# Kernel optimization log

Hardware: AMD Instinct MI355X
Metric: run time of the kernel (lower is better)

Reference implementation:

```python
import jax, jax.numpy as jnp
import numpy as np


def setup_inputs() -> dict:
    key = jax.random.key(0)
    ks = jax.random.split(key, 4)
    B, H, W, C = 4, 64, 64, 256
    Ck = C // 8
    x = jax.random.normal(ks[0], (B, H, W, C), dtype=jnp.float32)
    Wf = jax.random.normal(ks[1], (C, Ck), dtype=jnp.float32) * (1.0 / np.sqrt(C))
    Wg = jax.random.normal(ks[2], (C, Ck), dtype=jnp.float32) * (1.0 / np.sqrt(C))
    Wh = jax.random.normal(ks[3], (C, C), dtype=jnp.float32) * (1.0 / np.sqrt(C))
    bf = jnp.zeros((Ck,), jnp.float32)
    bg = jnp.zeros((Ck,), jnp.float32)
    bh = jnp.zeros((C,), jnp.float32)
    gamma = jnp.ones((1,), jnp.float32)
    return {"x": x, "Wf": Wf, "bf": bf, "Wg": Wg, "bg": bg, "Wh": Wh, "bh": bh, "gamma": gamma}


def reference(x, Wf, bf, Wg, bg, Wh, bh, gamma):
    B, H, W, C = x.shape
    N = H * W
    xf = x.reshape(B, N, C)  # hw_flatten; 1x1 conv == per-pixel matmul
    f = xf @ Wf + bf          # [B, N, C//8] (keys)
    g = xf @ Wg + bg          # [B, N, C//8] (queries)
    h = xf @ Wh + bh          # [B, N, C]    (values)
    s = jnp.einsum('bnk,bmk->bnm', g, f)   # [B, N, N], no scaling (as in source)
    b = jax.nn.softmax(s, axis=-1)
    o = jnp.einsum('bnm,bmc->bnc', b, h)   # [B, N, C]
    y = gamma * o.reshape(B, H, W, C) + x
    return y
```

## Files before the change

kernel.cpp:

```cpp
#include <hip/hip_runtime.h>
#include <stdint.h>

typedef short short8 __attribute__((ext_vector_type(8)));
typedef short short4_t __attribute__((ext_vector_type(4)));
typedef float f32x4 __attribute__((ext_vector_type(4)));

__device__ __forceinline__ float bf2f(unsigned short u) {
    union { unsigned int i; float f; } v; v.i = ((unsigned int)u) << 16; return v.f;
}
__device__ __forceinline__ unsigned short f2bf(float f) {
    union { float f; unsigned int i; } v; v.f = f;
    return (unsigned short)((v.i + 0x8000u) >> 16);
}

__global__ __launch_bounds__(256) void k_pre(const float* __restrict__ x,
                                             const float* __restrict__ Wf,
                                             const float* __restrict__ Wg,
                                             const float* __restrict__ Wh,
                                             unsigned short* __restrict__ xh,
                                             unsigned short* __restrict__ xl,
                                             unsigned short* __restrict__ wTh,
                                             unsigned short* __restrict__ wTl) {
    if (blockIdx.x < 2048) {
        int gid = blockIdx.x * 256 + threadIdx.x;
        const float* src = x + (size_t)gid * 8;
        f32x4 a0 = *(const f32x4*)src;
        f32x4 a1 = *(const f32x4*)(src + 4);
        short8 sh, sl;
#pragma unroll
        for (int j = 0; j < 4; ++j) {
            unsigned short h0 = f2bf(a0[j]);
            sh[j] = (short)h0; sl[j] = (short)f2bf(a0[j] - bf2f(h0));
            unsigned short h1 = f2bf(a1[j]);
            sh[4 + j] = (short)h1; sl[4 + j] = (short)f2bf(a1[j] - bf2f(h1));
        }
        *(short8*)&xh[(size_t)gid * 8] = sh;
        *(short8*)&xl[(size_t)gid * 8] = sl;
    } else {
        int col = blockIdx.x - 2048;
        int k = threadIdx.x;
        float v;
        if (col < 32) v = Wf[k * 32 + col];
        else if (col < 64) v = Wg[k * 32 + (col - 32)];
        else v = Wh[k * 256 + (col - 64)];
        unsigned short h = f2bf(v);
        wTh[col * 256 + k] = h;
        if (col < 64) wTl[col * 256 + k] = f2bf(v - bf2f(h));
    }
}

__global__ __launch_bounds__(256) void k_proj(
    const unsigned short* __restrict__ xh,
    const unsigned short* __restrict__ xl,
    const unsigned short* __restrict__ wTh,
    const unsigned short* __restrict__ wTl,
    const float* __restrict__ bfb,
    const float* __restrict__ bgb,
    const float* __restrict__ bhb,
    unsigned short* __restrict__ fKh,
    unsigned short* __restrict__ fKl,
    unsigned short* __restrict__ gQh,
    unsigned short* __restrict__ gQl,
    unsigned short* __restrict__ hT) {
    __shared__ short sm[4 * 64 * 72];
    int tid = threadIdx.x;
    int wave = tid >> 6, lane = tid & 63, lq = lane & 15, quad = lane >> 4;
    int rt = blockIdx.x;
    const unsigned short* xhb = xh + (size_t)rt * 64 * 256;
    const unsigned short* xlb = xl + (size_t)rt * 64 * 256;
    f32x4 zero4 = {0.f, 0.f, 0.f, 0.f};

    if (blockIdx.y < 4) {
        const int XO = 0, WO = 64 * 136;
        int cb = blockIdx.y;
        const unsigned short* wbase = wTh + (size_t)(64 + cb * 64) * 256;
        f32x4 acc[4] = {zero4, zero4, zero4, zero4};

        for (int ph = 0; ph < 2; ++ph) {
            int k0 = ph * 128;
            __syncthreads();
#pragma unroll
            for (int u = 0; u < 4; ++u) {
                int q = u * 256 + tid;
                int row = q >> 4, kc = q & 15;
                *(short8*)&sm[XO + row * 136 + kc * 8] =
                    *(const short8*)&xhb[row * 256 + k0 + kc * 8];
                *(short8*)&sm[WO + row * 136 + kc * 8] =
                    *(const short8*)&wbase[row * 256 + k0 + kc * 8];
            }
            __syncthreads();
#pragma unroll
            for (int ks = 0; ks < 4; ++ks) {
                short8 a = *(const short8*)&sm[XO + (wave * 16 + lq) * 136 + ks * 32 + quad * 8];
#pragma unroll
                for (int ct = 0; ct < 4; ++ct) {
                    short8 bfr = *(const short8*)&sm[WO + (lq + 16 * ct) * 136 + ks * 32 + quad * 8];
                    acc[ct] = __builtin_amdgcn_mfma_f32_16x16x32_bf16(a, bfr, acc[ct], 0, 0, 0);
                }
            }
        }

        int rowl = wave * 16 + quad * 4;
        int grow0 = rt * 64;
        int bidx = grow0 >> 12, n0 = (grow0 & 4095) + rowl;
#pragma unroll
        for (int ct = 0; ct < 4; ++ct) {
            int c = cb * 64 + lq + 16 * ct;
            float bias = bhb[c];
            short4_t pk;
#pragma unroll
            for (int r = 0; r < 4; ++r) pk[r] = (short)f2bf(acc[ct][r] + bias);
            size_t a8 = (((size_t)(bidx * 16 + (c >> 4)) * 128 + (n0 >> 5)) * 64 +
                         ((n0 & 31) >> 3) * 16 + (c & 15)) * 8 + (n0 & 7);
            *(short4_t*)&hT[a8] = pk;
        }
    } else {
        const int XH = 0, XL = 64 * 72, WH = 2 * 64 * 72, WL = 3 * 64 * 72;
        f32x4 acc[4] = {zero4, zero4, zero4, zero4};

        for (int ph = 0; ph < 4; ++ph) {
            int k0 = ph * 64;
            __syncthreads();
#pragma unroll
            for (int u = 0; u < 2; ++u) {
                int q = u * 256 + tid;
                int row = q >> 3, kc = q & 7;
                *(short8*)&sm[XH + row * 72 + kc * 8] =
                    *(const short8*)&xhb[row * 256 + k0 + kc * 8];
                *(short8*)&sm[XL + row * 72 + kc * 8] =
                    *(const short8*)&xlb[row * 256 + k0 + kc * 8];
                *(short8*)&sm[WH + row * 72 + kc * 8] =
                    *(const short8*)&wTh[row * 256 + k0 + kc * 8];
                *(short8*)&sm[WL + row * 72 + kc * 8] =
                    *(const short8*)&wTl[row * 256 + k0 + kc * 8];
            }
            __syncthreads();
#pragma unroll
            for (int ks = 0; ks < 2; ++ks) {
                short8 ah = *(const short8*)&sm[XH + (wave * 16 + lq) * 72 + ks * 32 + quad * 8];
                short8 al = *(const short8*)&sm[XL + (wave * 16 + lq) * 72 + ks * 32 + quad * 8];
#pragma unroll
                for (int ct = 0; ct < 4; ++ct) {
                    short8 bh = *(const short8*)&sm[WH + (lq + 16 * ct) * 72 + ks * 32 + quad * 8];
                    short8 bl = *(const short8*)&sm[WL + (lq + 16 * ct) * 72 + ks * 32 + quad * 8];
                    acc[ct] = __builtin_amdgcn_mfma_f32_16x16x32_bf16(ah, bh, acc[ct], 0, 0, 0);
                    acc[ct] = __builtin_amdgcn_mfma_f32_16x16x32_bf16(al, bh, acc[ct], 0, 0, 0);
                    acc[ct] = __builtin_amdgcn_mfma_f32_16x16x32_bf16(ah, bl, acc[ct], 0, 0, 0);
                }
            }
        }

        int rowl = wave * 16 + quad * 4;
#pragma unroll
        for (int ct = 0; ct < 4; ++ct) {
            int coll = lq + 16 * ct;
#pragma unroll
            for (int r = 0; r < 4; ++r) {
                int grow = rt * 64 + rowl + r;
                int bidx = grow >> 12, n = grow & 4095;
                float v = acc[ct][r];
                size_t o = (size_t)(bidx * 256 + (n >> 4)) * 512 +
                           (((coll & 31) >> 3) * 16 + (n & 15)) * 8 + (coll & 7);
                if (coll < 32) {
                    v += bfb[coll];
                    unsigned short h = f2bf(v);
                    fKh[o] = h;
                    fKl[o] = f2bf(v - bf2f(h));
                } else {
                    int cg = coll - 32;
                    size_t og = (size_t)(bidx * 256 + (n >> 4)) * 512 +
                                ((cg >> 3) * 16 + (n & 15)) * 8 + (cg & 7);
                    v += bgb[cg];
                    unsigned short h = f2bf(v);
                    gQh[og] = h;
                    gQl[og] = f2bf(v - bf2f(h));
                }
            }
        }
    }
}

#define PSTR 72
__global__ __launch_bounds__(256, 2) void k_attn(
    const unsigned short* __restrict__ fKh,
    const unsigned short* __restrict__ fKl,
    const unsigned short* __restrict__ gQh,
    const unsigned short* __restrict__ gQl,
    const unsigned short* __restrict__ hT,
    float* __restrict__ pacc0,
    float* __restrict__ pacc1,
    float* __restrict__ pl0,
    float* __restrict__ pl1) {
    __shared__ short Ps[2][64 * PSTR];
    __shared__ short Fb[2][2][2048];
    int tid = threadIdx.x;
    int wave = tid >> 6, lane = tid & 63, lq = lane & 15, quad = lane >> 4;
    int b = blockIdx.x & 3;
    int rest = blockIdx.x >> 2;
    int qt = rest & 63;
    int ks = rest >> 6;

    const unsigned short* fhB = fKh + (size_t)b * 131072;
    const unsigned short* flB = fKl + (size_t)b * 131072;
    const unsigned short* hB  = hT + (size_t)b * 1048576;
    float* pacc = ks ? pacc1 : pacc0;
    float* pl   = ks ? pl1 : pl0;

    int qrow0 = qt * 64 + wave * 16;
    int lchunk = quad * 16 + lq;

    f32x4 zero4 = {0.f, 0.f, 0.f, 0.f};
    f32x4 acc[16];
#pragma unroll
    for (int i = 0; i < 16; ++i) acc[i] = zero4;
    float l_part[4] = {0.f, 0.f, 0.f, 0.f};

    int gtile = b * 256 + qt * 4 + wave;
    short8 ghfrag = *(const short8*)&gQh[(size_t)gtile * 512 + lchunk * 8];
    short8 glfrag = *(const short8*)&gQl[(size_t)gtile * 512 + lchunk * 8];

    int ft0 = ks * 128;
    *(short8*)&Fb[0][0][tid * 8] = *(const short8*)&fhB[(size_t)ft0 * 512 + tid * 8];
    *(short8*)&Fb[0][1][tid * 8] = *(const short8*)&flB[(size_t)ft0 * 512 + tid * 8];
    __syncthreads();

    for (int kt = 0; kt < 32; ++kt) {
        int p = kt & 1;
        int nft = ft0 + (kt < 31 ? (kt + 1) * 4 : kt * 4);
        short8 fnh = *(const short8*)&fhB[(size_t)nft * 512 + tid * 8];
        short8 fnl = *(const short8*)&flB[(size_t)nft * 512 + tid * 8];

        int k0 = ks * 64 + kt * 2;
        short8 hb[4][2];
#pragma unroll
        for (int ct = 0; ct < 4; ++ct) {
            int ctile = wave * 4 + ct;
#pragma unroll
            for (int kk = 0; kk < 2; ++kk)
                hb[ct][kk] = *(const short8*)
                    &hB[(((size_t)ctile * 128 + k0 + kk) * 64 + lchunk) * 8];
        }

        f32x4 S[4];
#pragma unroll
        for (int t = 0; t < 4; ++t) {
            short8 fh = *(const short8*)&Fb[p][0][t * 512 + lchunk * 8];
            short8 fl = *(const short8*)&Fb[p][1][t * 512 + lchunk * 8];
            S[t] = __builtin_amdgcn_mfma_f32_16x16x32_bf16(ghfrag, fh, zero4, 0, 0, 0);
            S[t] = __builtin_amdgcn_mfma_f32_16x16x32_bf16(glfrag, fh, S[t], 0, 0, 0);
            S[t] = __builtin_amdgcn_mfma_f32_16x16x32_bf16(ghfrag, fl, S[t], 0, 0, 0);
        }

#pragma unroll
        for (int t = 0; t < 4; ++t)
#pragma unroll
            for (int r = 0; r < 4; ++r) S[t][r] = __expf(S[t][r]);
#pragma unroll
        for (int r = 0; r < 4; ++r)
            l_part[r] += (S[0][r] + S[1][r]) + (S[2][r] + S[3][r]);

#pragma unroll
        for (int t = 0; t < 4; ++t)
#pragma unroll
            for (int r = 0; r < 4; ++r)
                Ps[p][(wave * 16 + quad * 4 + r) * PSTR + lq + 16 * t] =
                    (short)f2bf(S[t][r]);

        *(short8*)&Fb[1 - p][0][tid * 8] = fnh;
        *(short8*)&Fb[1 - p][1][tid * 8] = fnl;

        __syncthreads();

#pragma unroll
        for (int rb = 0; rb < 4; ++rb) {
            short8 pa0 = *(const short8*)&Ps[p][(rb * 16 + lq) * PSTR + quad * 8];
            short8 pa1 = *(const short8*)&Ps[p][(rb * 16 + lq) * PSTR + 32 + quad * 8];
#pragma unroll
            for (int ct = 0; ct < 4; ++ct) {
                acc[rb * 4 + ct] = __builtin_amdgcn_mfma_f32_16x16x32_bf16(pa0, hb[ct][0], acc[rb * 4 + ct], 0, 0, 0);
                acc[rb * 4 + ct] = __builtin_amdgcn_mfma_f32_16x16x32_bf16(pa1, hb[ct][1], acc[rb * 4 + ct], 0, 0, 0);
            }
        }
    }

#pragma unroll
    for (int r = 0; r < 4; ++r) {
        float s = l_part[r];
        s += __shfl_xor(s, 1);
        s += __shfl_xor(s, 2);
        s += __shfl_xor(s, 4);
        s += __shfl_xor(s, 8);
        if (lq == 0)
            pl[b * 4096 + qrow0 + quad * 4 + r] = s;
    }
#pragma unroll
    for (int rb = 0; rb < 4; ++rb)
#pragma unroll
        for (int ct = 0; ct < 4; ++ct) {
            int c = wave * 64 + ct * 16 + lq;
#pragma unroll
            for (int r = 0; r < 4; ++r) {
                int n = qt * 64 + rb * 16 + quad * 4 + r;
                pacc[((size_t)(b * 4096 + n)) * 256 + c] = acc[rb * 4 + ct][r];
            }
        }
}

__global__ __launch_bounds__(256) void k_combine(
    const float* __restrict__ x,
    const float* __restrict__ gam_p,
    const float* __restrict__ pacc1,
    const float* __restrict__ pl0,
    const float* __restrict__ pl1,
    float* __restrict__ out) {
    int gid = blockIdx.x * 256 + threadIdx.x;
    int row = gid >> 6;
    f32x4 a0 = *(const f32x4*)&out[(size_t)gid * 4];
    f32x4 a1 = *(const f32x4*)&pacc1[(size_t)gid * 4];
    f32x4 xv = *(const f32x4*)&x[(size_t)gid * 4];
    float linv = 1.0f / (pl0[row] + pl1[row]);
    float gam = gam_p[0];
    f32x4 o;
#pragma unroll
    for (int j = 0; j < 4; ++j) o[j] = gam * ((a0[j] + a1[j]) * linv) + xv[j];
    *(f32x4*)&out[(size_t)gid * 4] = o;
}

extern "C" void kernel_launch(void* const* d_in, const int* in_sizes, int n_in,
                              void* d_out, int out_size, void* d_ws, size_t ws_size,
                              hipStream_t stream) {
    const float* x   = (const float*)d_in[0];
    const float* Wf  = (const float*)d_in[1];
    const float* bfb = (const float*)d_in[2];
    const float* Wg  = (const float*)d_in[3];
    const float* bgb = (const float*)d_in[4];
    const float* Wh  = (const float*)d_in[5];
    const float* bhb = (const float*)d_in[6];
    const float* gam = (const float*)d_in[7];
    float* out = (float*)d_out;

    char* ws = (char*)d_ws;
    const size_t MI = 1u << 20;
    unsigned short* xh  = (unsigned short*)(ws);
    unsigned short* xl  = (unsigned short*)(ws + 8 * MI);
    unsigned short* fKh = (unsigned short*)(ws + 16 * MI);
    unsigned short* fKl = (unsigned short*)(ws + 17 * MI);
    unsigned short* gQh = (unsigned short*)(ws + 18 * MI);
    unsigned short* gQl = (unsigned short*)(ws + 19 * MI);
    unsigned short* hT  = (unsigned short*)(ws + 20 * MI);
    unsigned short* wTh = (unsigned short*)(ws + 28 * MI);
    unsigned short* wTl = (unsigned short*)(ws + 28 * MI + 160 * 1024);
    float* pacc1 = (float*)(ws + 29 * MI);
    float* pl0   = (float*)(ws + 45 * MI);
    float* pl1   = (float*)(ws + 45 * MI + 64 * 1024);

    k_pre<<<dim3(2368), dim3(256), 0, stream>>>(x, Wf, Wg, Wh, xh, xl, wTh, wTl);
    k_proj<<<dim3(256, 5), dim3(256), 0, stream>>>(xh, xl, wTh, wTl, bfb, bgb, bhb,
                                                   fKh, fKl, gQh, gQl, hT);
    k_attn<<<dim3(512), dim3(256), 0, stream>>>(fKh, fKl, gQh, gQl, hT,
                                                out, pacc1, pl0, pl1);
    k_combine<<<dim3(4096), dim3(256), 0, stream>>>(x, gam, pacc1, pl0, pl1, out);
}
```

Before: 153.0 us.

## Restructure attention blocks to 32 query rows, 8 waves, fused epilogue without split-K

Replaces the two-way split over keys plus a separate combine kernel with one attention kernel per 32-query tile using 512 threads, where each wave computes one 16x16 score tile and a 16x32 slice of the output. The softmax denominator is reduced through shared memory and the normalization, gamma scaling and residual add are done in the epilogue, removing the partial-accumulator round trip through global memory and the extra launch. It also adds s_setprio around MFMA sections. In exchange, the h-value tiles are reloaded for each 32-row tile rather than each 64-row tile, which doubles that global traffic, and each block now loops over all keys.

After: 152.0 us. No clear change (-0.6%).

```diff
diff --git a/kernel.cpp b/kernel.cpp
--- a/kernel.cpp
+++ b/kernel.cpp
@@ -181,106 +181,98 @@
 }
 
 #define PSTR 72
-__global__ __launch_bounds__(256, 2) void k_attn(
+__global__ __launch_bounds__(512, 4) void k_attn(
     const unsigned short* __restrict__ fKh,
     const unsigned short* __restrict__ fKl,
     const unsigned short* __restrict__ gQh,
     const unsigned short* __restrict__ gQl,
     const unsigned short* __restrict__ hT,
-    float* __restrict__ pacc0,
-    float* __restrict__ pacc1,
-    float* __restrict__ pl0,
-    float* __restrict__ pl1) {
-    __shared__ short Ps[2][64 * PSTR];
+    const float* __restrict__ x,
+    const float* __restrict__ gam_p,
+    float* __restrict__ out) {
+    __shared__ short Ps[2][32 * PSTR];
     __shared__ short Fb[2][2][2048];
+    __shared__ float Lred[2][16][4];
     int tid = threadIdx.x;
     int wave = tid >> 6, lane = tid & 63, lq = lane & 15, quad = lane >> 4;
     int b = blockIdx.x & 3;
-    int rest = blockIdx.x >> 2;
-    int qt = rest & 63;
-    int ks = rest >> 6;
+    int qt = blockIdx.x >> 2;
+    int rs = wave >> 2;
+    int kt4 = wave & 3;
 
     const unsigned short* fhB = fKh + (size_t)b * 131072;
     const unsigned short* flB = fKl + (size_t)b * 131072;
     const unsigned short* hB  = hT + (size_t)b * 1048576;
-    float* pacc = ks ? pacc1 : pacc0;
-    float* pl   = ks ? pl1 : pl0;
-
-    int qrow0 = qt * 64 + wave * 16;
     int lchunk = quad * 16 + lq;
 
     f32x4 zero4 = {0.f, 0.f, 0.f, 0.f};
-    f32x4 acc[16];
-#pragma unroll
-    for (int i = 0; i < 16; ++i) acc[i] = zero4;
+    f32x4 acc[4];
+#pragma unroll
+    for (int i = 0; i < 4; ++i) acc[i] = zero4;
     float l_part[4] = {0.f, 0.f, 0.f, 0.f};
 
-    int gtile = b * 256 + qt * 4 + wave;
+    int gtile = b * 256 + qt * 2 + rs;
     short8 ghfrag = *(const short8*)&gQh[(size_t)gtile * 512 + lchunk * 8];
     short8 glfrag = *(const short8*)&gQl[(size_t)gtile * 512 + lchunk * 8];
 
-    int ft0 = ks * 128;
-    *(short8*)&Fb[0][0][tid * 8] = *(const short8*)&fhB[(size_t)ft0 * 512 + tid * 8];
-    *(short8*)&Fb[0][1][tid * 8] = *(const short8*)&flB[(size_t)ft0 * 512 + tid * 8];
+    int sid = tid & 255;
+    int hl = tid >> 8;
+    const unsigned short* fB0 = hl ? flB : fhB;
+
+    *(short8*)&Fb[0][hl][sid * 8] = *(const short8*)&fB0[(size_t)sid * 8];
     __syncthreads();
 
-    for (int kt = 0; kt < 32; ++kt) {
+    for (int kt = 0; kt < 64; ++kt) {
         int p = kt & 1;
-        int nft = ft0 + (kt < 31 ? (kt + 1) * 4 : kt * 4);
-        short8 fnh = *(const short8*)&fhB[(size_t)nft * 512 + tid * 8];
-        short8 fnl = *(const short8*)&flB[(size_t)nft * 512 + tid * 8];
-
-        int k0 = ks * 64 + kt * 2;
-        short8 hb[4][2];
-#pragma unroll
-        for (int ct = 0; ct < 4; ++ct) {
-            int ctile = wave * 4 + ct;
+        int nkt = kt < 63 ? kt + 1 : kt;
+        short8 fn = *(const short8*)&fB0[(size_t)nkt * 2048 + sid * 8];
+
+        int k0 = kt * 2;
+        short8 hb[2][2];
+#pragma unroll
+        for (int ct = 0; ct < 2; ++ct) {
+            int ctile = wave * 2 + ct;
 #pragma unroll
             for (int kk = 0; kk < 2; ++kk)
                 hb[ct][kk] = *(const short8*)
                     &hB[(((size_t)ctile * 128 + k0 + kk) * 64 + lchunk) * 8];
         }
 
-        f32x4 S[4];
-#pragma unroll
-        for (int t = 0; t < 4; ++t) {
-            short8 fh = *(const short8*)&Fb[p][0][t * 512 + lchunk * 8];
-            short8 fl = *(const short8*)&Fb[p][1][t * 512 + lchunk * 8];
-            S[t] = __builtin_amdgcn_mfma_f32_16x16x32_bf16(ghfrag, fh, zero4, 0, 0, 0);
-            S[t] = __builtin_amdgcn_mfma_f32_16x16x32_bf16(glfrag, fh, S[t], 0, 0, 0);
-            S[t] = __builtin_amdgcn_mfma_f32_16x16x32_bf16(ghfrag, fl, S[t], 0, 0, 0);
-        }
-
-#pragma unroll
-        for (int t = 0; t < 4; ++t)
-#pragma unroll
-            for (int r = 0; r < 4; ++r) S[t][r] = __expf(S[t][r]);
+        short8 fh = *(const short8*)&Fb[p][0][kt4 * 512 + lchunk * 8];
+        short8 fl = *(const short8*)&Fb[p][1][kt4 * 512 + lchunk * 8];
+        __builtin_amdgcn_s_setprio(1);
+        f32x4 S = __builtin_amdgcn_mfma_f32_16x16x32_bf16(ghfrag, fh, zero4, 0, 0, 0);
+        S = __builtin_amdgcn_mfma_f32_16x16x32_bf16(glfrag, fh, S, 0, 0, 0);
+        S = __builtin_amdgcn_mfma_f32_16x16x32_bf16(ghfrag, fl, S, 0, 0, 0);
+        __builtin_amdgcn_s_setprio(0);
+
+#pragma unroll
+        for (int r = 0; r < 4; ++r) {
+            S[r] = __expf(S[r]);
+            l_part[r] += S[r];
+        }
+
 #pragma unroll
         for (int r = 0; r < 4; ++r)
-            l_part[r] += (S[0][r] + S[1][r]) + (S[2][r] + S[3][r]);
-
-#pragma unroll
-        for (int t = 0; t < 4; ++t)
-#pragma unroll
-            for (int r = 0; r < 4; ++r)
-                Ps[p][(wave * 16 + quad * 4 + r) * PSTR + lq + 16 * t] =
-                    (short)f2bf(S[t][r]);
-
-        *(short8*)&Fb[1 - p][0][tid * 8] = fnh;
-        *(short8*)&Fb[1 - p][1][tid * 8] = fnl;
+            Ps[p][(rs * 16 + quad * 4 + r) * PSTR + kt4 * 16 + lq] =
+                (short)f2bf(S[r]);
+
+        *(short8*)&Fb[1 - p][hl][sid * 8] = fn;
 
         __syncthreads();
 
-#pragma unroll
-        for (int rb = 0; rb < 4; ++rb) {
+        __builtin_amdgcn_s_setprio(1);
+#pragma unroll
+        for (int rb = 0; rb < 2; ++rb) {
             short8 pa0 = *(const short8*)&Ps[p][(rb * 16 + lq) * PSTR + quad * 8];
             short8 pa1 = *(const short8*)&Ps[p][(rb * 16 + lq) * PSTR + 32 + quad * 8];
 #pragma unroll
-            for (int ct = 0; ct < 4; ++ct) {
-                acc[rb * 4 + ct] = __builtin_amdgcn_mfma_f32_16x16x32_bf16(pa0, hb[ct][0], acc[rb * 4 + ct], 0, 0, 0);
-                acc[rb * 4 + ct] = __builtin_amdgcn_mfma_f32_16x16x32_bf16(pa1, hb[ct][1], acc[rb * 4 + ct], 0, 0, 0);
-            }
-        }
+            for (int ct = 0; ct < 2; ++ct) {
+                acc[rb * 2 + ct] = __builtin_amdgcn_mfma_f32_16x16x32_bf16(pa0, hb[ct][0], acc[rb * 2 + ct], 0, 0, 0);
+                acc[rb * 2 + ct] = __builtin_amdgcn_mfma_f32_16x16x32_bf16(pa1, hb[ct][1], acc[rb * 2 + ct], 0, 0, 0);
+            }
+        }
+        __builtin_amdgcn_s_setprio(0);
     }
 
 #pragma unroll
@@ -290,40 +282,26 @@
         s += __shfl_xor(s, 2);
         s += __shfl_xor(s, 4);
         s += __shfl_xor(s, 8);
-        if (lq == 0)
-            pl[b * 4096 + qrow0 + quad * 4 + r] = s;
+        if (lq == 0) Lred[rs][quad * 4 + r][kt4] = s;
     }
-#pragma unroll
-    for (int rb = 0; rb < 4; ++rb)
-#pragma unroll
-        for (int ct = 0; ct < 4; ++ct) {
-            int c = wave * 64 + ct * 16 + lq;
-#pragma unroll
-            for (int r = 0; r < 4; ++r) {
-                int n = qt * 64 + rb * 16 + quad * 4 + r;
-                pacc[((size_t)(b * 4096 + n)) * 256 + c] = acc[rb * 4 + ct][r];
-            }
-        }
-}
-
-__global__ __launch_bounds__(256) void k_combine(
-    const float* __restrict__ x,
-    const float* __restrict__ gam_p,
-    const float* __restrict__ pacc1,
-    const float* __restrict__ pl0,
-    const float* __restrict__ pl1,
-    float* __restrict__ out) {
-    int gid = blockIdx.x * 256 + threadIdx.x;
-    int row = gid >> 6;
-    f32x4 a0 = *(const f32x4*)&out[(size_t)gid * 4];
-    f32x4 a1 = *(const f32x4*)&pacc1[(size_t)gid * 4];
-    f32x4 xv = *(const f32x4*)&x[(size_t)gid * 4];
-    float linv = 1.0f / (pl0[row] + pl1[row]);
+    __syncthreads();
+
     float gam = gam_p[0];
-    f32x4 o;
-#pragma unroll
-    for (int j = 0; j < 4; ++j) o[j] = gam * ((a0[j] + a1[j]) * linv) + xv[j];
-    *(f32x4*)&out[(size_t)gid * 4] = o;
+#pragma unroll
+    for (int rb = 0; rb < 2; ++rb)
+#pragma unroll
+        for (int r = 0; r < 4; ++r) {
+            float l = Lred[rb][quad * 4 + r][0] + Lred[rb][quad * 4 + r][1] +
+                      Lred[rb][quad * 4 + r][2] + Lred[rb][quad * 4 + r][3];
+            float linv = 1.0f / l;
+            int n = qt * 32 + rb * 16 + quad * 4 + r;
+            size_t rowo = ((size_t)(b * 4096 + n)) * 256;
+#pragma unroll
+            for (int ct = 0; ct < 2; ++ct) {
+                int c = wave * 32 + ct * 16 + lq;
+                out[rowo + c] = gam * (acc[rb * 2 + ct][r] * linv) + x[rowo + c];
+            }
+        }
 }
 
 extern "C" void kernel_launch(void* const* d_in, const int* in_sizes, int n_in,
@@ -350,14 +328,10 @@
     unsigned short* hT  = (unsigned short*)(ws + 20 * MI);
     unsigned short* wTh = (unsigned short*)(ws + 28 * MI);
     unsigned short* wTl = (unsigned short*)(ws + 28 * MI + 160 * 1024);
-    float* pacc1 = (float*)(ws + 29 * MI);
-    float* pl0   = (float*)(ws + 45 * MI);
-    float* pl1   = (float*)(ws + 45 * MI + 64 * 1024);
 
     k_pre<<<dim3(2368), dim3(256), 0, stream>>>(x, Wf, Wg, Wh, xh, xl, wTh, wTl);
     k_proj<<<dim3(256, 5), dim3(256), 0, stream>>>(xh, xl, wTh, wTl, bfb, bgb, bhb,
                                                    fKh, fKl, gQh, gQl, hT);
-    k_attn<<<dim3(512), dim3(256), 0, stream>>>(fKh, fKl, gQh, gQl, hT,
-                                                out, pacc1, pl0, pl1);
-    k_combine<<<dim3(4096), dim3(256), 0, stream>>>(x, gam, pacc1, pl0, pl1, out);
-}
+    k_attn<<<dim3(512), dim3(512), 0, stream>>>(fKh, fKl, gQh, gQl, hT,
+                                                x, gam, out);
+}
```

## Fuse split-K combine into attention kernel via atomic flags and widen key tile

Applied to the files above, without the earlier changes.

Removes the separate combine kernel. Each pair of split-K blocks writes its partial results and an atomic counter marks completion, so the second block to finish merges both halves, normalizes, applies gamma and adds the residual in place. The key tile per iteration doubles from 64 to 128 (16 iterations instead of 32), halving the number of barriers, and s_setprio is raised around the MFMA sections. This costs more LDS and registers per block, which may hurt occupancy, and adds a memset launch plus atomics and fences.

Measured after the change: 254.4 us. 66.3% more time.

```diff
diff --git a/kernel.cpp b/kernel.cpp
--- a/kernel.cpp
+++ b/kernel.cpp
@@ -180,34 +180,34 @@
     }
 }
 
-#define PSTR 72
+#define PSTR 136
 __global__ __launch_bounds__(256, 2) void k_attn(
     const unsigned short* __restrict__ fKh,
     const unsigned short* __restrict__ fKl,
     const unsigned short* __restrict__ gQh,
     const unsigned short* __restrict__ gQl,
     const unsigned short* __restrict__ hT,
-    float* __restrict__ pacc0,
+    const float* __restrict__ x,
+    const float* __restrict__ gam_p,
+    float* __restrict__ out,
     float* __restrict__ pacc1,
-    float* __restrict__ pl0,
-    float* __restrict__ pl1) {
+    float* __restrict__ pl,
+    int* __restrict__ flags) {
     __shared__ short Ps[2][64 * PSTR];
-    __shared__ short Fb[2][2][2048];
+    __shared__ short Fb[2][2][4096];
+    __shared__ float Lql[64];
+    __shared__ int tick_s;
     int tid = threadIdx.x;
     int wave = tid >> 6, lane = tid & 63, lq = lane & 15, quad = lane >> 4;
     int b = blockIdx.x & 3;
     int rest = blockIdx.x >> 2;
     int qt = rest & 63;
     int ks = rest >> 6;
+    int lchunk = quad * 16 + lq;
 
     const unsigned short* fhB = fKh + (size_t)b * 131072;
     const unsigned short* flB = fKl + (size_t)b * 131072;
     const unsigned short* hB  = hT + (size_t)b * 1048576;
-    float* pacc = ks ? pacc1 : pacc0;
-    float* pl   = ks ? pl1 : pl0;
-
-    int qrow0 = qt * 64 + wave * 16;
-    int lchunk = quad * 16 + lq;
 
     f32x4 zero4 = {0.f, 0.f, 0.f, 0.f};
     f32x4 acc[16];
@@ -219,68 +219,83 @@
     short8 ghfrag = *(const short8*)&gQh[(size_t)gtile * 512 + lchunk * 8];
     short8 glfrag = *(const short8*)&gQl[(size_t)gtile * 512 + lchunk * 8];
 
-    int ft0 = ks * 128;
-    *(short8*)&Fb[0][0][tid * 8] = *(const short8*)&fhB[(size_t)ft0 * 512 + tid * 8];
-    *(short8*)&Fb[0][1][tid * 8] = *(const short8*)&flB[(size_t)ft0 * 512 + tid * 8];
+    int ft_base = ks * 65536;
+
+    *(short8*)&Fb[0][0][tid * 8]        = *(const short8*)&fhB[ft_base + tid * 8];
+    *(short8*)&Fb[0][0][2048 + tid * 8] = *(const short8*)&fhB[ft_base + 2048 + tid * 8];
+    *(short8*)&Fb[0][1][tid * 8]        = *(const short8*)&flB[ft_base + tid * 8];
+    *(short8*)&Fb[0][1][2048 + tid * 8] = *(const short8*)&flB[ft_base + 2048 + tid * 8];
     __syncthreads();
 
-    for (int kt = 0; kt < 32; ++kt) {
-        int p = kt & 1;
-        int nft = ft0 + (kt < 31 ? (kt + 1) * 4 : kt * 4);
-        short8 fnh = *(const short8*)&fhB[(size_t)nft * 512 + tid * 8];
-        short8 fnl = *(const short8*)&flB[(size_t)nft * 512 + tid * 8];
-
-        int k0 = ks * 64 + kt * 2;
-        short8 hb[4][2];
+    for (int t = 0; t < 16; ++t) {
+        int p = t & 1;
+        size_t gn = (size_t)ft_base + (size_t)(t < 15 ? t + 1 : t) * 4096;
+        short8 fn0 = *(const short8*)&fhB[gn + tid * 8];
+        short8 fn1 = *(const short8*)&fhB[gn + 2048 + tid * 8];
+        short8 fn2 = *(const short8*)&flB[gn + tid * 8];
+        short8 fn3 = *(const short8*)&flB[gn + 2048 + tid * 8];
+
+        int k0 = ks * 64 + t * 4;
+        short8 hb[4][4];
 #pragma unroll
         for (int ct = 0; ct < 4; ++ct) {
             int ctile = wave * 4 + ct;
 #pragma unroll
-            for (int kk = 0; kk < 2; ++kk)
+            for (int kk = 0; kk < 4; ++kk)
                 hb[ct][kk] = *(const short8*)
                     &hB[(((size_t)ctile * 128 + k0 + kk) * 64 + lchunk) * 8];
         }
 
-        f32x4 S[4];
-#pragma unroll
-        for (int t = 0; t < 4; ++t) {
-            short8 fh = *(const short8*)&Fb[p][0][t * 512 + lchunk * 8];
-            short8 fl = *(const short8*)&Fb[p][1][t * 512 + lchunk * 8];
-            S[t] = __builtin_amdgcn_mfma_f32_16x16x32_bf16(ghfrag, fh, zero4, 0, 0, 0);
-            S[t] = __builtin_amdgcn_mfma_f32_16x16x32_bf16(glfrag, fh, S[t], 0, 0, 0);
-            S[t] = __builtin_amdgcn_mfma_f32_16x16x32_bf16(ghfrag, fl, S[t], 0, 0, 0);
-        }
-
-#pragma unroll
-        for (int t = 0; t < 4; ++t)
-#pragma unroll
-            for (int r = 0; r < 4; ++r) S[t][r] = __expf(S[t][r]);
-#pragma unroll
-        for (int r = 0; r < 4; ++r)
-            l_part[r] += (S[0][r] + S[1][r]) + (S[2][r] + S[3][r]);
-
-#pragma unroll
-        for (int t = 0; t < 4; ++t)
+        f32x4 S[8];
+        __builtin_amdgcn_s_setprio(1);
+#pragma unroll
+        for (int u = 0; u < 8; ++u) {
+            short8 fh = *(const short8*)&Fb[p][0][u * 512 + lchunk * 8];
+            short8 fl = *(const short8*)&Fb[p][1][u * 512 + lchunk * 8];
+            S[u] = __builtin_amdgcn_mfma_f32_16x16x32_bf16(ghfrag, fh, zero4, 0, 0, 0);
+            S[u] = __builtin_amdgcn_mfma_f32_16x16x32_bf16(glfrag, fh, S[u], 0, 0, 0);
+            S[u] = __builtin_amdgcn_mfma_f32_16x16x32_bf16(ghfrag, fl, S[u], 0, 0, 0);
+        }
+        __builtin_amdgcn_s_setprio(0);
+
+#pragma unroll
+        for (int u = 0; u < 8; ++u)
+#pragma unroll
+            for (int r = 0; r < 4; ++r) {
+                float e = __expf(S[u][r]);
+                S[u][r] = e;
+                l_part[r] += e;
+            }
+
+#pragma unroll
+        for (int u = 0; u < 8; ++u)
 #pragma unroll
             for (int r = 0; r < 4; ++r)
-                Ps[p][(wave * 16 + quad * 4 + r) * PSTR + lq + 16 * t] =
-                    (short)f2bf(S[t][r]);
-
-        *(short8*)&Fb[1 - p][0][tid * 8] = fnh;
-        *(short8*)&Fb[1 - p][1][tid * 8] = fnl;
+                Ps[p][(wave * 16 + quad * 4 + r) * PSTR + u * 16 + lq] =
+                    (short)f2bf(S[u][r]);
+
+        *(short8*)&Fb[1 - p][0][tid * 8] = fn0;
+        *(short8*)&Fb[1 - p][0][2048 + tid * 8] = fn1;
+        *(short8*)&Fb[1 - p][1][tid * 8] = fn2;
+        *(short8*)&Fb[1 - p][1][2048 + tid * 8] = fn3;
 
         __syncthreads();
 
+        __builtin_amdgcn_s_setprio(1);
 #pragma unroll
         for (int rb = 0; rb < 4; ++rb) {
-            short8 pa0 = *(const short8*)&Ps[p][(rb * 16 + lq) * PSTR + quad * 8];
-            short8 pa1 = *(const short8*)&Ps[p][(rb * 16 + lq) * PSTR + 32 + quad * 8];
-#pragma unroll
-            for (int ct = 0; ct < 4; ++ct) {
-                acc[rb * 4 + ct] = __builtin_amdgcn_mfma_f32_16x16x32_bf16(pa0, hb[ct][0], acc[rb * 4 + ct], 0, 0, 0);
-                acc[rb * 4 + ct] = __builtin_amdgcn_mfma_f32_16x16x32_bf16(pa1, hb[ct][1], acc[rb * 4 + ct], 0, 0, 0);
-            }
-        }
+            short8 pa[4];
+#pragma unroll
+            for (int kk = 0; kk < 4; ++kk)
+                pa[kk] = *(const short8*)&Ps[p][(rb * 16 + lq) * PSTR + kk * 32 + quad * 8];
+#pragma unroll
+            for (int kk = 0; kk < 4; ++kk)
+#pragma unroll
+                for (int ct = 0; ct < 4; ++ct)
+                    acc[rb * 4 + ct] = __builtin_amdgcn_mfma_f32_16x16x32_bf16(
+                        pa[kk], hb[ct][kk], acc[rb * 4 + ct], 0, 0, 0);
+        }
+        __builtin_amdgcn_s_setprio(0);
     }
 
 #pragma unroll
@@ -290,9 +305,13 @@
         s += __shfl_xor(s, 2);
         s += __shfl_xor(s, 4);
         s += __shfl_xor(s, 8);
-        if (lq == 0)
-            pl[b * 4096 + qrow0 + quad * 4 + r] = s;
+        if (lq == 0) Lql[wave * 16 + quad * 4 + r] = s;
     }
+    __syncthreads();
+
+    int pair = b * 64 + qt;
+    size_t pbase = (size_t)pair * 64 * 256;
+    float* mypart = ks ? pacc1 : out;
 #pragma unroll
     for (int rb = 0; rb < 4; ++rb)
 #pragma unroll
@@ -300,30 +319,36 @@
             int c = wave * 64 + ct * 16 + lq;
 #pragma unroll
             for (int r = 0; r < 4; ++r) {
-                int n = qt * 64 + rb * 16 + quad * 4 + r;
-                pacc[((size_t)(b * 4096 + n)) * 256 + c] = acc[rb * 4 + ct][r];
-            }
-        }
-}
-
-__global__ __launch_bounds__(256) void k_combine(
-    const float* __restrict__ x,
-    const float* __restrict__ gam_p,
-    const float* __restrict__ pacc1,
-    const float* __restrict__ pl0,
-    const float* __restrict__ pl1,
-    float* __restrict__ out) {
-    int gid = blockIdx.x * 256 + threadIdx.x;
-    int row = gid >> 6;
-    f32x4 a0 = *(const f32x4*)&out[(size_t)gid * 4];
-    f32x4 a1 = *(const f32x4*)&pacc1[(size_t)gid * 4];
-    f32x4 xv = *(const f32x4*)&x[(size_t)gid * 4];
-    float linv = 1.0f / (pl0[row] + pl1[row]);
+                int n = rb * 16 + quad * 4 + r;
+                mypart[pbase + (size_t)n * 256 + c] = acc[rb * 4 + ct][r];
+            }
+        }
+    if (tid < 64) pl[(size_t)(ks * 256 + pair) * 64 + tid] = Lql[tid];
+
+    __threadfence();
+    __syncthreads();
+    if (tid == 0) tick_s = atomicAdd(&flags[pair], 1);
+    __syncthreads();
+    if (tick_s == 0) return;
+    __threadfence();
+
+    const float* opart = ks ? out : pacc1;
+    const float* plp = &pl[(size_t)((1 - ks) * 256 + pair) * 64];
     float gam = gam_p[0];
-    f32x4 o;
-#pragma unroll
-    for (int j = 0; j < 4; ++j) o[j] = gam * ((a0[j] + a1[j]) * linv) + xv[j];
-    *(f32x4*)&out[(size_t)gid * 4] = o;
+#pragma unroll
+    for (int rb = 0; rb < 4; ++rb)
+#pragma unroll
+        for (int r = 0; r < 4; ++r) {
+            int n = rb * 16 + quad * 4 + r;
+            float linv = 1.0f / (Lql[n] + plp[n]);
+            size_t rowo = pbase + (size_t)n * 256;
+#pragma unroll
+            for (int ct = 0; ct < 4; ++ct) {
+                int c = wave * 64 + ct * 16 + lq;
+                float o = acc[rb * 4 + ct][r] + opart[rowo + c];
+                out[rowo + c] = gam * o * linv + x[rowo + c];
+            }
+        }
 }
 
 extern "C" void kernel_launch(void* const* d_in, const int* in_sizes, int n_in,
@@ -351,13 +376,13 @@
     unsigned short* wTh = (unsigned short*)(ws + 28 * MI);
     unsigned short* wTl = (unsigned short*)(ws + 28 * MI + 160 * 1024);
     float* pacc1 = (float*)(ws + 29 * MI);
-    float* pl0   = (float*)(ws + 45 * MI);
-    float* pl1   = (float*)(ws + 45 * MI + 64 * 1024);
-
+    float* pl    = (float*)(ws + 45 * MI);
+    int*   flags = (int*)(ws + 45 * MI + 128 * 1024);
+
+    hipMemsetAsync(flags, 0, 256 * sizeof(int), stream);
     k_pre<<<dim3(2368), dim3(256), 0, stream>>>(x, Wf, Wg, Wh, xh, xl, wTh, wTl);
     k_proj<<<dim3(256, 5), dim3(256), 0, stream>>>(xh, xl, wTh, wTl, bfb, bgb, bhb,
                                                    fKh, fKl, gQh, gQl, hT);
     k_attn<<<dim3(512), dim3(256), 0, stream>>>(fKh, fKl, gQh, gQl, hT,
-                                                out, pacc1, pl0, pl1);
-    k_combine<<<dim3(4096), dim3(256), 0, stream>>>(x, gam, pacc1, pl0, pl1, out);
-}
+                                                x, gam, out, pacc1, pl, flags);
+}
```
